# Performance work log

Measured on AMD Instinct MI355X. Metric: run time of the kernel, lower is better.

## Reference

```python
import jax, jax.numpy as jnp
import numpy as np

EMBED = 1024
HEADS = 16
HEAD_DIM = EMBED // HEADS


def setup_inputs() -> dict:
    key = jax.random.key(0)
    ks = jax.random.split(key, 6)
    scale = 1.0 / np.sqrt(EMBED)
    x = jax.random.normal(ks[0], (2, 2048, EMBED), dtype=jnp.float32)
    # nn.Linear weights stored as [out_features, in_features]
    Wq = jax.random.normal(ks[1], (EMBED, EMBED), dtype=jnp.float32) * scale
    Wk = jax.random.normal(ks[2], (EMBED, EMBED), dtype=jnp.float32) * scale
    Wv = jax.random.normal(ks[3], (EMBED, EMBED), dtype=jnp.float32) * scale
    Wo = jax.random.normal(ks[4], (EMBED, EMBED), dtype=jnp.float32) * scale
    bo = jax.random.normal(ks[5], (EMBED,), dtype=jnp.float32) * scale
    return {"x": x, "Wq": Wq, "Wk": Wk, "Wv": Wv, "Wo": Wo, "bo": bo}


def reference(x, Wq, Wk, Wv, Wo, bo):
    N, L, E = x.shape
    # projections (torch Linear: x @ W.T)
    q = (x @ Wq.T).reshape(N, L, HEADS, HEAD_DIM).transpose(0, 2, 1, 3)  # [N,H,L,D]
    k = (x @ Wk.T).reshape(N, L, HEADS, HEAD_DIM).transpose(0, 2, 1, 3)
    v = (x @ Wv.T).reshape(N, L, HEADS, HEAD_DIM).transpose(0, 2, 1, 3)
    # scores scaled by sqrt(embed_size) (as in source, not sqrt(head_dim))
    scores = jnp.einsum("nhqd,nhkd->nhqk", q, k) / jnp.sqrt(jnp.float32(E))
    attn = jax.nn.softmax(scores, axis=-1)
    out = jnp.einsum("nhqk,nhkd->nhqd", attn, v)  # [N,H,L,D]
    out = out.transpose(0, 2, 1, 3).reshape(N, L, E)
    return out @ Wo.T + bo
```

## Files before the change

### kernel.cpp

```cpp
#include <hip/hip_runtime.h>
#include <hip/hip_bf16.h>

constexpr int NB  = 2;
constexpr int SL  = 2048;
constexpr int EMB = 1024;
constexpr int NH  = 16;
constexpr int HD  = 64;
constexpr int MT  = NB * SL;
constexpr size_t PROJ = (size_t)MT * EMB;

typedef __attribute__((ext_vector_type(8))) short bf16x8;
typedef __attribute__((ext_vector_type(4))) float f32x4;

__device__ inline short f2b(float f) {
  __hip_bfloat16 b = __float2bfloat16(f);
  short s; __builtin_memcpy(&s, &b, 2); return s;
}

#define GLDS16(g, l)                                                     \
  __builtin_amdgcn_global_load_lds(                                      \
      (const __attribute__((address_space(1))) void*)(g),                \
      (__attribute__((address_space(3))) void*)(l), 16, 0, 0)

__global__ __launch_bounds__(256) void cast_all(
    const float* __restrict__ x,  const float* __restrict__ wq,
    const float* __restrict__ wk, const float* __restrict__ wv,
    const float* __restrict__ wo, short* __restrict__ xb,
    short* __restrict__ wqkv, short* __restrict__ wob) {
  const size_t t = (size_t)blockIdx.x * 256 + threadIdx.x;
  const float* src; short* dst; size_t base;
  if (t < 1048576)      { src = x;  dst = xb;              base = 0; }
  else if (t < 1310720) { src = wq; dst = wqkv;            base = 1048576; }
  else if (t < 1572864) { src = wk; dst = wqkv + (1 << 20); base = 1310720; }
  else if (t < 1835008) { src = wv; dst = wqkv + (2 << 20); base = 1572864; }
  else                  { src = wo; dst = wob;             base = 1835008; }
  const size_t i = t - base;
  const float4 v = ((const float4*)src)[i];
  const short4 o = {f2b(v.x), f2b(v.y), f2b(v.z), f2b(v.w)};
  ((short4*)dst)[i] = o;
}

template <int MODE>
__global__ __launch_bounds__(256) void gemm_mfma(
    const short* __restrict__ A, const short* __restrict__ W,
    const float* __restrict__ bias, short* __restrict__ qb,
    short* __restrict__ kb, short* __restrict__ vt, float* __restrict__ out) {
  __shared__ short As[128 * 32];
  __shared__ short Bs[128 * 32];
  const int tid = threadIdx.x;
  const int w = tid >> 6, lane = tid & 63;
  const int la = lane >> 4, lb = lane & 15;
  const int wm = w & 1, wn = w >> 1;
  const int m0 = blockIdx.y << 7, n0 = blockIdx.x << 7;
  const int srow = lane >> 2, scol = (lane & 3) << 3;
  const short* a0 = A + (size_t)(m0 + w * 16 + srow) * 1024 + scol;
  const short* b0 = W + (size_t)(n0 + w * 16 + srow) * 1024 + scol;
  short* lA0 = As + (w * 16) * 32;
  short* lA1 = As + (64 + w * 16) * 32;
  short* lB0 = Bs + (w * 16) * 32;
  short* lB1 = Bs + (64 + w * 16) * 32;

  f32x4 acc[4][4];
#pragma unroll
  for (int i = 0; i < 4; ++i)
#pragma unroll
    for (int j = 0; j < 4; ++j) acc[i][j] = (f32x4){0.f, 0.f, 0.f, 0.f};

  for (int k0 = 0; k0 < 1024; k0 += 32) {
    __syncthreads();
    GLDS16(a0 + k0, lA0);
    GLDS16(a0 + 64 * 1024 + k0, lA1);
    GLDS16(b0 + k0, lB0);
    GLDS16(b0 + 64 * 1024 + k0, lB1);
    __syncthreads();
    bf16x8 af[4], bf[4];
#pragma unroll
    for (int i = 0; i < 4; ++i)
      af[i] = *(const bf16x8*)&As[(wm * 64 + i * 16 + lb) * 32 + la * 8];
#pragma unroll
    for (int j = 0; j < 4; ++j)
      bf[j] = *(const bf16x8*)&Bs[(wn * 64 + j * 16 + lb) * 32 + la * 8];
#pragma unroll
    for (int i = 0; i < 4; ++i)
#pragma unroll
      for (int j = 0; j < 4; ++j)
        acc[i][j] = __builtin_amdgcn_mfma_f32_16x16x32_bf16(af[i], bf[j],
                                                            acc[i][j], 0, 0, 0);
  }

  if (MODE == 1) {
#pragma unroll
    for (int j = 0; j < 4; ++j) {
      const int nj = n0 + wn * 64 + j * 16 + lb;
      const float bv = bias[nj];
#pragma unroll
      for (int i = 0; i < 4; ++i) {
        const int mi = m0 + wm * 64 + i * 16 + la * 4;
#pragma unroll
        for (int r = 0; r < 4; ++r)
          out[(size_t)(mi + r) * 1024 + nj] = acc[i][j][r] + bv;
      }
    }
  } else {
    const int region = n0 >> 10;
    if (region < 2) {
      short* dst = region ? kb : qb;
      const float sc = region ? 1.0f : 0.03125f;
      const int nb0 = n0 & 1023;
#pragma unroll
      for (int j = 0; j < 4; ++j) {
        const int nj = nb0 + wn * 64 + j * 16 + lb;
#pragma unroll
        for (int i = 0; i < 4; ++i) {
          const int mi = m0 + wm * 64 + i * 16 + la * 4;
#pragma unroll
          for (int r = 0; r < 4; ++r)
            dst[(size_t)(mi + r) * 1024 + nj] = f2b(acc[i][j][r] * sc);
        }
      }
    } else {
#pragma unroll
      for (int j = 0; j < 4; ++j) {
        const int nv = (n0 - 2048) + wn * 64 + j * 16 + lb;
        const int h = nv >> 6, d = nv & 63;
#pragma unroll
        for (int i = 0; i < 4; ++i) {
          const int mi = m0 + wm * 64 + i * 16 + la * 4;
          const int nbi = mi >> 11, seq = mi & (SL - 1);
          const int k5 = seq & 31;
          const int seqp = (seq & ~31) | (8 * ((k5 >> 2) & 3) + 4 * (k5 >> 4));
          const short4 o = {f2b(acc[i][j][0]), f2b(acc[i][j][1]),
                            f2b(acc[i][j][2]), f2b(acc[i][j][3])};
          *(short4*)&vt[((size_t)(nbi * NH + h) * HD + d) * SL + seqp] = o;
        }
      }
    }
  }
}

__global__ __launch_bounds__(256, 2) void attn_mfma(const short* __restrict__ Qg,
                                                    const short* __restrict__ Kg,
                                                    const short* __restrict__ Vtg,
                                                    short* __restrict__ Ab) {
  __shared__ short Qs[128][72];
  __shared__ short Ks[64][72];
  __shared__ short Vt[64][72];
  const int tid = threadIdx.x;
  const int wv = tid >> 6, lane = tid & 63;
  const int G = lane >> 4, lb = lane & 15;
  const int qt = blockIdx.x, h = blockIdx.y, n = blockIdx.z;
  const int qbase = qt << 7;

  {
    const short* Qb = Qg + ((size_t)(n * SL + qbase)) * EMB + h * HD;
    const int row = tid >> 3, c = (tid & 7) << 3;
#pragma unroll
    for (int k = 0; k < 4; ++k)
      *(bf16x8*)&Qs[row + 32 * k][c] =
          *(const bf16x8*)(Qb + (size_t)(row + 32 * k) * EMB + c);
  }

  f32x4 O[4][2];
  float l[2] = {0.f, 0.f};
#pragma unroll
  for (int mt = 0; mt < 4; ++mt)
#pragma unroll
    for (int nt = 0; nt < 2; ++nt) O[mt][nt] = (f32x4){0.f, 0.f, 0.f, 0.f};

  for (int kt = 0; kt < SL / 64; ++kt) {
    __syncthreads();
    const short* Kb = Kg + ((size_t)(n * SL + (kt << 6))) * EMB + h * HD;
    const short* Vb = Vtg + ((size_t)(n * NH + h)) * HD * SL + (kt << 6);
    const int row = tid >> 3, c = (tid & 7) << 3;
#pragma unroll
    for (int k = 0; k < 2; ++k) {
      *(bf16x8*)&Ks[row + 32 * k][c] =
          *(const bf16x8*)(Kb + (size_t)(row + 32 * k) * EMB + c);
      *(bf16x8*)&Vt[row + 32 * k][c] =
          *(const bf16x8*)(Vb + (size_t)(row + 32 * k) * SL + c);
    }
    __syncthreads();

    f32x4 S[4][2];
#pragma unroll
    for (int mt = 0; mt < 4; ++mt)
#pragma unroll
      for (int nt = 0; nt < 2; ++nt) S[mt][nt] = (f32x4){0.f, 0.f, 0.f, 0.f};
#pragma unroll
    for (int ks = 0; ks < 2; ++ks) {
      bf16x8 aK[4], bQ[2];
#pragma unroll
      for (int mt = 0; mt < 4; ++mt)
        aK[mt] = *(const bf16x8*)&Ks[16 * mt + lb][32 * ks + 8 * G];
#pragma unroll
      for (int nt = 0; nt < 2; ++nt)
        bQ[nt] = *(const bf16x8*)&Qs[32 * wv + 16 * nt + lb][32 * ks + 8 * G];
#pragma unroll
      for (int mt = 0; mt < 4; ++mt)
#pragma unroll
        for (int nt = 0; nt < 2; ++nt)
          S[mt][nt] = __builtin_amdgcn_mfma_f32_16x16x32_bf16(aK[mt], bQ[nt],
                                                              S[mt][nt], 0, 0, 0);
    }

#pragma unroll
    for (int nt = 0; nt < 2; ++nt) {
      float ls = 0.f;
#pragma unroll
      for (int mt = 0; mt < 4; ++mt)
#pragma unroll
        for (int r = 0; r < 4; ++r) {
          const float p = __expf(S[mt][nt][r]);
          S[mt][nt][r] = p;
          ls += p;
        }
      ls += __shfl_xor(ls, 16);
      ls += __shfl_xor(ls, 32);
      l[nt] += ls;
    }

#pragma unroll
    for (int s = 0; s < 2; ++s) {
      bf16x8 aV[4];
#pragma unroll
      for (int mt = 0; mt < 4; ++mt)
        aV[mt] = *(const bf16x8*)&Vt[16 * mt + lb][32 * s + 8 * G];
#pragma unroll
      for (int nt = 0; nt < 2; ++nt) {
        bf16x8 B2;
        B2[0] = f2b(S[2 * s][nt][0]);
        B2[1] = f2b(S[2 * s][nt][1]);
        B2[2] = f2b(S[2 * s][nt][2]);
        B2[3] = f2b(S[2 * s][nt][3]);
        B2[4] = f2b(S[2 * s + 1][nt][0]);
        B2[5] = f2b(S[2 * s + 1][nt][1]);
        B2[6] = f2b(S[2 * s + 1][nt][2]);
        B2[7] = f2b(S[2 * s + 1][nt][3]);
#pragma unroll
        for (int mt = 0; mt < 4; ++mt)
          O[mt][nt] = __builtin_amdgcn_mfma_f32_16x16x32_bf16(aV[mt], B2,
                                                              O[mt][nt], 0, 0, 0);
      }
    }
  }

  short* Ao = Ab + ((size_t)(n * SL + qbase)) * EMB + h * HD;
#pragma unroll
  for (int nt = 0; nt < 2; ++nt) {
    const float inv = 1.f / l[nt];
    const int q = 32 * wv + 16 * nt + lb;
#pragma unroll
    for (int mt = 0; mt < 4; ++mt) {
      const short4 o = {f2b(O[mt][nt][0] * inv), f2b(O[mt][nt][1] * inv),
                        f2b(O[mt][nt][2] * inv), f2b(O[mt][nt][3] * inv)};
      *(short4*)(Ao + (size_t)q * EMB + 16 * mt + 4 * G) = o;
    }
  }
}

extern "C" void kernel_launch(void* const* d_in, const int* in_sizes, int n_in,
                              void* d_out, int out_size, void* d_ws, size_t ws_size,
                              hipStream_t stream) {
  const float* x  = (const float*)d_in[0];
  const float* Wq = (const float*)d_in[1];
  const float* Wk = (const float*)d_in[2];
  const float* Wv = (const float*)d_in[3];
  const float* Wo = (const float*)d_in[4];
  const float* bo = (const float*)d_in[5];
  float* out = (float*)d_out;

  short* xb   = (short*)d_ws;
  short* wqkv = xb + PROJ;
  short* wob  = wqkv + 3u * EMB * EMB;
  short* qb   = wob + (size_t)EMB * EMB;
  short* kb   = qb + PROJ;
  short* vt   = kb + PROJ;
  short* ab   = qb;

  cast_all<<<8192, 256, 0, stream>>>(x, Wq, Wk, Wv, Wo, xb, wqkv, wob);
  gemm_mfma<0><<<dim3(24, 32), 256, 0, stream>>>(xb, wqkv, nullptr, qb, kb, vt,
                                                 nullptr);
  attn_mfma<<<dim3(SL / 128, NH, NB), 256, 0, stream>>>(qb, kb, vt, ab);
  gemm_mfma<1><<<dim3(8, 32), 256, 0, stream>>>(ab, wob, bo, nullptr, nullptr,
                                                nullptr, out);
}
```

Baseline: 194.0 us.

## Prefetch K/V tiles in registers, hoist Q fragments, use exp2, split output GEMM

The attention loop now prefetches the next K/V tile into registers while computing the current one, and loads Q fragments once instead of on every iteration. Softmax uses exp2 with log2(e) folded into the Q scale. The output projection gets its own kernel with 128x64 tiles, giving 512 blocks instead of 256 to fill the CUs better. The costs are extra registers in attention, which may hurt occupancy, and less B reuse per block in the output GEMM.

```diff
diff --git a/kernel.cpp b/kernel.cpp
--- a/kernel.cpp
+++ b/kernel.cpp
@@ -40,11 +40,9 @@
   ((short4*)dst)[i] = o;
 }
 
-template <int MODE>
-__global__ __launch_bounds__(256) void gemm_mfma(
+__global__ __launch_bounds__(256) void gemm_qkv(
     const short* __restrict__ A, const short* __restrict__ W,
-    const float* __restrict__ bias, short* __restrict__ qb,
-    short* __restrict__ kb, short* __restrict__ vt, float* __restrict__ out) {
+    short* __restrict__ qb, short* __restrict__ kb, short* __restrict__ vt) {
   __shared__ short As[128 * 32];
   __shared__ short Bs[128 * 32];
   const int tid = threadIdx.x;
@@ -88,52 +86,94 @@
                                                             acc[i][j], 0, 0, 0);
   }
 
-  if (MODE == 1) {
+  const int region = n0 >> 10;
+  if (region < 2) {
+    short* dst = region ? kb : qb;
+    const float sc = region ? 1.0f : 0.03125f * 1.44269504f;
+    const int nb0 = n0 & 1023;
 #pragma unroll
     for (int j = 0; j < 4; ++j) {
-      const int nj = n0 + wn * 64 + j * 16 + lb;
-      const float bv = bias[nj];
+      const int nj = nb0 + wn * 64 + j * 16 + lb;
 #pragma unroll
       for (int i = 0; i < 4; ++i) {
         const int mi = m0 + wm * 64 + i * 16 + la * 4;
 #pragma unroll
         for (int r = 0; r < 4; ++r)
-          out[(size_t)(mi + r) * 1024 + nj] = acc[i][j][r] + bv;
+          dst[(size_t)(mi + r) * 1024 + nj] = f2b(acc[i][j][r] * sc);
       }
     }
   } else {
-    const int region = n0 >> 10;
-    if (region < 2) {
-      short* dst = region ? kb : qb;
-      const float sc = region ? 1.0f : 0.03125f;
-      const int nb0 = n0 & 1023;
-#pragma unroll
-      for (int j = 0; j < 4; ++j) {
-        const int nj = nb0 + wn * 64 + j * 16 + lb;
-#pragma unroll
-        for (int i = 0; i < 4; ++i) {
-          const int mi = m0 + wm * 64 + i * 16 + la * 4;
-#pragma unroll
-          for (int r = 0; r < 4; ++r)
-            dst[(size_t)(mi + r) * 1024 + nj] = f2b(acc[i][j][r] * sc);
-        }
+#pragma unroll
+    for (int j = 0; j < 4; ++j) {
+      const int nv = (n0 - 2048) + wn * 64 + j * 16 + lb;
+      const int h = nv >> 6, d = nv & 63;
+#pragma unroll
+      for (int i = 0; i < 4; ++i) {
+        const int mi = m0 + wm * 64 + i * 16 + la * 4;
+        const int nbi = mi >> 11, seq = mi & (SL - 1);
+        const int k5 = seq & 31;
+        const int seqp = (seq & ~31) | (8 * ((k5 >> 2) & 3) + 4 * (k5 >> 4));
+        const short4 o = {f2b(acc[i][j][0]), f2b(acc[i][j][1]),
+                          f2b(acc[i][j][2]), f2b(acc[i][j][3])};
+        *(short4*)&vt[((size_t)(nbi * NH + h) * HD + d) * SL + seqp] = o;
       }
-    } else {
-#pragma unroll
-      for (int j = 0; j < 4; ++j) {
-        const int nv = (n0 - 2048) + wn * 64 + j * 16 + lb;
-        const int h = nv >> 6, d = nv & 63;
-#pragma unroll
-        for (int i = 0; i < 4; ++i) {
-          const int mi = m0 + wm * 64 + i * 16 + la * 4;
-          const int nbi = mi >> 11, seq = mi & (SL - 1);
-          const int k5 = seq & 31;
-          const int seqp = (seq & ~31) | (8 * ((k5 >> 2) & 3) + 4 * (k5 >> 4));
-          const short4 o = {f2b(acc[i][j][0]), f2b(acc[i][j][1]),
-                            f2b(acc[i][j][2]), f2b(acc[i][j][3])};
-          *(short4*)&vt[((size_t)(nbi * NH + h) * HD + d) * SL + seqp] = o;
-        }
-      }
+    }
+  }
+}
+
+__global__ __launch_bounds__(256) void gemm_out(
+    const short* __restrict__ A, const short* __restrict__ W,
+    const float* __restrict__ bias, float* __restrict__ out) {
+  __shared__ short As[128 * 32];
+  __shared__ short Bs[64 * 32];
+  const int tid = threadIdx.x;
+  const int w = tid >> 6, lane = tid & 63;
+  const int la = lane >> 4, lb = lane & 15;
+  const int wm = w & 1, wn = w >> 1;
+  const int m0 = blockIdx.y << 7, n0 = blockIdx.x << 6;
+  const int srow = lane >> 2, scol = (lane & 3) << 3;
+  const short* a0 = A + (size_t)(m0 + w * 16 + srow) * 1024 + scol;
+  const short* b0 = W + (size_t)(n0 + w * 16 + srow) * 1024 + scol;
+  short* lA0 = As + (w * 16) * 32;
+  short* lA1 = As + (64 + w * 16) * 32;
+  short* lB0 = Bs + (w * 16) * 32;
+
+  f32x4 acc[4][2];
+#pragma unroll
+  for (int i = 0; i < 4; ++i)
+#pragma unroll
+    for (int j = 0; j < 2; ++j) acc[i][j] = (f32x4){0.f, 0.f, 0.f, 0.f};
+
+  for (int k0 = 0; k0 < 1024; k0 += 32) {
+    __syncthreads();
+    GLDS16(a0 + k0, lA0);
+    GLDS16(a0 + 64 * 1024 + k0, lA1);
+    GLDS16(b0 + k0, lB0);
+    __syncthreads();
+    bf16x8 af[4], bf[2];
+#pragma unroll
+    for (int i = 0; i < 4; ++i)
+      af[i] = *(const bf16x8*)&As[(wm * 64 + i * 16 + lb) * 32 + la * 8];
+#pragma unroll
+    for (int j = 0; j < 2; ++j)
+      bf[j] = *(const bf16x8*)&Bs[(wn * 32 + j * 16 + lb) * 32 + la * 8];
+#pragma unroll
+    for (int i = 0; i < 4; ++i)
+#pragma unroll
+      for (int j = 0; j < 2; ++j)
+        acc[i][j] = __builtin_amdgcn_mfma_f32_16x16x32_bf16(af[i], bf[j],
+                                                            acc[i][j], 0, 0, 0);
+  }
+#pragma unroll
+  for (int j = 0; j < 2; ++j) {
+    const int nj = n0 + wn * 32 + j * 16 + lb;
+    const float bv = bias[nj];
+#pragma unroll
+    for (int i = 0; i < 4; ++i) {
+      const int mi = m0 + wm * 64 + i * 16 + la * 4;
+#pragma unroll
+      for (int r = 0; r < 4; ++r)
+        out[(size_t)(mi + r) * 1024 + nj] = acc[i][j][r] + bv;
     }
   }
 }
@@ -150,15 +190,22 @@
   const int G = lane >> 4, lb = lane & 15;
   const int qt = blockIdx.x, h = blockIdx.y, n = blockIdx.z;
   const int qbase = qt << 7;
+  const int row = tid >> 3, c = (tid & 7) << 3;
 
   {
     const short* Qb = Qg + ((size_t)(n * SL + qbase)) * EMB + h * HD;
-    const int row = tid >> 3, c = (tid & 7) << 3;
 #pragma unroll
     for (int k = 0; k < 4; ++k)
       *(bf16x8*)&Qs[row + 32 * k][c] =
           *(const bf16x8*)(Qb + (size_t)(row + 32 * k) * EMB + c);
   }
+  __syncthreads();
+  bf16x8 bQ[2][2];
+#pragma unroll
+  for (int nt = 0; nt < 2; ++nt)
+#pragma unroll
+    for (int ks = 0; ks < 2; ++ks)
+      bQ[nt][ks] = *(const bf16x8*)&Qs[32 * wv + 16 * nt + lb][32 * ks + 8 * G];
 
   f32x4 O[4][2];
   float l[2] = {0.f, 0.f};
@@ -167,19 +214,33 @@
 #pragma unroll
     for (int nt = 0; nt < 2; ++nt) O[mt][nt] = (f32x4){0.f, 0.f, 0.f, 0.f};
 
+  const short* Kb0 = Kg + ((size_t)(n * SL)) * EMB + h * HD;
+  const short* Vb0 = Vtg + ((size_t)(n * NH + h)) * HD * SL;
+
+  bf16x8 pk[2], pv[2];
+#pragma unroll
+  for (int k = 0; k < 2; ++k) {
+    pk[k] = *(const bf16x8*)(Kb0 + (size_t)(row + 32 * k) * EMB + c);
+    pv[k] = *(const bf16x8*)(Vb0 + (size_t)(row + 32 * k) * SL + c);
+  }
+
   for (int kt = 0; kt < SL / 64; ++kt) {
     __syncthreads();
-    const short* Kb = Kg + ((size_t)(n * SL + (kt << 6))) * EMB + h * HD;
-    const short* Vb = Vtg + ((size_t)(n * NH + h)) * HD * SL + (kt << 6);
-    const int row = tid >> 3, c = (tid & 7) << 3;
 #pragma unroll
     for (int k = 0; k < 2; ++k) {
-      *(bf16x8*)&Ks[row + 32 * k][c] =
-          *(const bf16x8*)(Kb + (size_t)(row + 32 * k) * EMB + c);
-      *(bf16x8*)&Vt[row + 32 * k][c] =
-          *(const bf16x8*)(Vb + (size_t)(row + 32 * k) * SL + c);
-    }
-    __syncthreads();
+      *(bf16x8*)&Ks[row + 32 * k][c] = pk[k];
+      *(bf16x8*)&Vt[row + 32 * k][c] = pv[k];
+    }
+    __syncthreads();
+    if (kt + 1 < SL / 64) {
+      const short* Kb = Kb0 + (size_t)(kt + 1) * 64 * EMB;
+      const short* Vb = Vb0 + (size_t)(kt + 1) * 64;
+#pragma unroll
+      for (int k = 0; k < 2; ++k) {
+        pk[k] = *(const bf16x8*)(Kb + (size_t)(row + 32 * k) * EMB + c);
+        pv[k] = *(const bf16x8*)(Vb + (size_t)(row + 32 * k) * SL + c);
+      }
+    }
 
     f32x4 S[4][2];
 #pragma unroll
@@ -188,18 +249,15 @@
       for (int nt = 0; nt < 2; ++nt) S[mt][nt] = (f32x4){0.f, 0.f, 0.f, 0.f};
 #pragma unroll
     for (int ks = 0; ks < 2; ++ks) {
-      bf16x8 aK[4], bQ[2];
+      bf16x8 aK[4];
 #pragma unroll
       for (int mt = 0; mt < 4; ++mt)
         aK[mt] = *(const bf16x8*)&Ks[16 * mt + lb][32 * ks + 8 * G];
 #pragma unroll
-      for (int nt = 0; nt < 2; ++nt)
-        bQ[nt] = *(const bf16x8*)&Qs[32 * wv + 16 * nt + lb][32 * ks + 8 * G];
-#pragma unroll
       for (int mt = 0; mt < 4; ++mt)
 #pragma unroll
         for (int nt = 0; nt < 2; ++nt)
-          S[mt][nt] = __builtin_amdgcn_mfma_f32_16x16x32_bf16(aK[mt], bQ[nt],
+          S[mt][nt] = __builtin_amdgcn_mfma_f32_16x16x32_bf16(aK[mt], bQ[nt][ks],
                                                               S[mt][nt], 0, 0, 0);
     }
 
@@ -210,7 +268,7 @@
       for (int mt = 0; mt < 4; ++mt)
 #pragma unroll
         for (int r = 0; r < 4; ++r) {
-          const float p = __expf(S[mt][nt][r]);
+          const float p = __builtin_amdgcn_exp2f(S[mt][nt][r]);
           S[mt][nt][r] = p;
           ls += p;
         }
@@ -278,9 +336,7 @@
   short* ab   = qb;
 
   cast_all<<<8192, 256, 0, stream>>>(x, Wq, Wk, Wv, Wo, xb, wqkv, wob);
-  gemm_mfma<0><<<dim3(24, 32), 256, 0, stream>>>(xb, wqkv, nullptr, qb, kb, vt,
-                                                 nullptr);
+  gemm_qkv<<<dim3(24, 32), 256, 0, stream>>>(xb, wqkv, qb, kb, vt);
   attn_mfma<<<dim3(SL / 128, NH, NB), 256, 0, stream>>>(qb, kb, vt, ab);
-  gemm_mfma<1><<<dim3(8, 32), 256, 0, stream>>>(ab, wob, bo, nullptr, nullptr,
-                                                nullptr, out);
-}
+  gemm_out<<<dim3(16, 32), 256, 0, stream>>>(ab, wob, bo, out);
+}
```

After: 179.4 us. 7.5% less time.
